# Kernel tuning notes

Hardware: AMD Instinct MI355X
Metric: run time of the kernel (lower is better)

## Reference

```python
import jax, jax.numpy as jnp
import numpy as np

B, S, UC = 64, 5, 50          # batch, sample (candidates), clicked history
D, T = 128, 768               # embedding_size, title_size
NE, NR, NN = 200000, 100, 50000  # entities, relations, news
K, A = 10, 20                 # neighbors per entity, anchor nodes per news


def _lin(k, out_d, in_d):
    w = jax.random.normal(k, (out_d, in_d), jnp.float32) * (1.0 / np.sqrt(in_d))
    b = jnp.zeros((out_d,), jnp.float32)
    return w, b


def setup_inputs() -> dict:
    key = jax.random.key(0)
    ks = jax.random.split(key, 16)
    W_nc1, b_nc1 = _lin(ks[0], D, T)
    W_nc2, b_nc2 = _lin(ks[1], D, D)
    W_anchor, b_anchor = _lin(ks[2], D, 2 * D)
    W_aw1, b_aw1 = _lin(ks[3], D, D)
    W_aw2, b_aw2 = _lin(ks[4], 1, D)
    W_mlp1, b_mlp1 = _lin(ks[5], D, 2 * D)
    W_mlp2, b_mlp2 = _lin(ks[6], D, D)
    return {
        "news_title_embedding": jax.random.normal(ks[7], (NN, T), jnp.float32),
        "entity_embedding": jax.random.normal(ks[8], (NE, D), jnp.float32),
        "relation_embedding": jax.random.normal(ks[9], (NR, D), jnp.float32),
        "W_nc1": W_nc1, "b_nc1": b_nc1, "W_nc2": W_nc2, "b_nc2": b_nc2,
        "W_anchor": W_anchor, "b_anchor": b_anchor,
        "W_aw1": W_aw1, "b_aw1": b_aw1, "W_aw2": W_aw2, "b_aw2": b_aw2,
        "W_mlp1": W_mlp1, "b_mlp1": b_mlp1, "W_mlp2": W_mlp2, "b_mlp2": b_mlp2,
        "cand_news": jax.random.randint(ks[10], (B, S), 0, NN, jnp.int32),
        "clicked_news": jax.random.randint(ks[11], (B, UC), 0, NN, jnp.int32),
        "cand_anchor_nodes": jax.random.randint(ks[12], (B * S, A), 0, NE, jnp.int32),
        "clicked_anchor_nodes": jax.random.randint(ks[13], (B * UC, A), 0, NE, jnp.int32),
        "entity_adj": jax.random.randint(ks[14], (NE, K), 0, NE, jnp.int32),
        "relation_adj": jax.random.randint(ks[15], (NE, K), 0, NR, jnp.int32),
    }


def reference(news_title_embedding, entity_embedding, relation_embedding,
              W_nc1, b_nc1, W_nc2, b_nc2,
              W_anchor, b_anchor, W_aw1, b_aw1, W_aw2, b_aw2,
              W_mlp1, b_mlp1, W_mlp2, b_mlp2,
              cand_news, clicked_news, cand_anchor_nodes, clicked_anchor_nodes,
              entity_adj, relation_adj):
    elu = jax.nn.elu

    def news_emb(ids_flat):  # [N] -> [N, D]
        t = news_title_embedding[ids_flat]                       # [N, T]
        return jnp.tanh(elu(t @ W_nc1.T + b_nc1) @ W_nc2.T + b_nc2)

    def anchor_graph_emb(nodes):  # [N, A] -> [N, D]
        node_e = entity_embedding[nodes]                          # [N, A, D]
        nb_ent = entity_embedding[entity_adj[nodes]]              # [N, A, K, D]
        nb_rel = relation_embedding[relation_adj[nodes]]          # [N, A, K, D]
        agg = jnp.sum(nb_ent + nb_rel, axis=-2)                   # [N, A, D]
        h = jnp.tanh(jnp.concatenate([node_e, agg], axis=-1) @ W_anchor.T + b_anchor)
        logits = elu(h @ W_aw1.T + b_aw1) @ W_aw2.T + b_aw2       # [N, A, 1]
        w = jax.nn.softmax(logits, axis=-2)                       # softmax over anchor nodes
        return jnp.sum(h * w, axis=-2)                            # [N, D]

    cand_e = news_emb(cand_news.reshape(-1))                      # [B*S, D]
    clk_e = news_emb(clicked_news.reshape(-1))                    # [B*UC, D]
    cand_e = jnp.concatenate([cand_e, anchor_graph_emb(cand_anchor_nodes)], axis=-1)
    clk_e = jnp.concatenate([clk_e, anchor_graph_emb(clicked_anchor_nodes)], axis=-1)

    def mlp(x):
        return elu(elu(x @ W_mlp1.T + b_mlp1) @ W_mlp2.T + b_mlp2)

    news_embedding = mlp(cand_e).reshape(B, S, -1)                # [B, S, D]
    user_embedding = jnp.mean(mlp(clk_e).reshape(B, UC, -1), axis=1)  # [B, D]
    score = jnp.sum(news_embedding * user_embedding[:, None, :], axis=-1)  # [B, S]
    return score
```

## Files before the change

kernel.cpp:

```cpp
#include <hip/hip_runtime.h>
#include <hip/hip_bf16.h>


#define B_ 64
#define S_ 5
#define UC_ 50
#define A_ 20
#define NCAND 320
#define NCLK 3200
#define NNEWS 3520
#define NANCH 70400

static constexpr long OFF_WNC1P = 64;
static constexpr long OFF_BNC1  = 98368;
static constexpr long OFF_WNC2P = 98496;
static constexpr long OFF_BNC2  = 114880;
static constexpr long OFF_WANCP = 115008;
static constexpr long OFF_BANC  = 147776;
static constexpr long OFF_WAW1P = 147904;
static constexpr long OFF_BAW1  = 164288;
static constexpr long OFF_WAW2  = 164416;
static constexpr long OFF_BAW2  = 164544;
static constexpr long OFF_WM1P  = 164548;
static constexpr long OFF_BM1   = 197316;
static constexpr long OFF_WM2P  = 197444;
static constexpr long OFF_BM2   = 213828;
static constexpr long OFF_REL   = 213956;
static constexpr long OFF_AE    = 226756;
static constexpr long OFF_NE    = 677316;
static constexpr long OFF_MO    = 1127876;

typedef __attribute__((ext_vector_type(8))) short short8v;
typedef __attribute__((ext_vector_type(4))) float f32x4;

__device__ __forceinline__ float ldf(const void* p, long i, int bf) {
  if (bf) {
    unsigned int u = (unsigned int)((const unsigned short*)p)[i];
    u <<= 16;
    return __uint_as_float(u);
  }
  return ((const float*)p)[i];
}

__device__ __forceinline__ float4 ldf4(const void* p, long i, int bf) {
  float4 f;
  if (bf) {
    const unsigned short* q = (const unsigned short*)p + i;
    uint2 u = *(const uint2*)q;
    f.x = __uint_as_float(u.x << 16);
    f.y = __uint_as_float(u.x & 0xffff0000u);
    f.z = __uint_as_float(u.y << 16);
    f.w = __uint_as_float(u.y & 0xffff0000u);
  } else {
    f = *(const float4*)((const float*)p + i);
  }
  return f;
}

__device__ __forceinline__ float eluf(float v) { return v > 0.f ? v : expm1f(v); }

__device__ __forceinline__ void splitbf(float v, unsigned short& hi, unsigned short& lo) {
  unsigned int b = __float_as_uint(v);
  hi = (unsigned short)(b >> 16);
  float rm = v - __uint_as_float(b & 0xffff0000u);
  unsigned int rb = __float_as_uint(rm);
  lo = (unsigned short)((rb + 0x7fffu + ((rb >> 16) & 1u)) >> 16);
}

__device__ __forceinline__ float bfh(unsigned short u) {
  return __uint_as_float((unsigned int)u << 16);
}

__global__ void k_detect(const void* ent, int* flag) {
  __shared__ int cnt;
  if (threadIdx.x == 0) cnt = 0;
  __syncthreads();
  unsigned short u = ((const unsigned short*)ent)[threadIdx.x];
  int e = (u >> 7) & 0xFF;
  int ok = (e >= 107 && e <= 146) ? 1 : 0;
  atomicAdd(&cnt, ok);
  __syncthreads();
  if (threadIdx.x == 0) *flag = (cnt >= 200) ? 1 : 0;
}

__global__ __launch_bounds__(256) void k_prep(
    const void* s0, const void* s1, const void* s2, const void* s3,
    const void* s4, const void* s5, const void* s6, const void* s7,
    const void* s8, const void* s9, const void* s10, const void* s11,
    const void* s12, const void* s13, const void* s14, float* ws) {
  const int bf = ((const int*)ws)[0];
  const void* srcs[15] = {s0,s1,s2,s3,s4,s5,s6,s7,s8,s9,s10,s11,s12,s13,s14};
  const int R[15] = {128,128,128,128,128,128,128,128,1,  1,  128,128,128,128,100};
  const int C[15] = {768,1,  128,1,  256,1,  128,1,  128,1,  256,1,  128,1,  128};
  const int MD[15]= {2,  0,  2,  0,  3,  0,  3,  0,  0,  0,  2,  0,  2,  0,  0};
  const long OFF[15] = {OFF_WNC1P,OFF_BNC1,OFF_WNC2P,OFF_BNC2,OFF_WANCP,OFF_BANC,
                        OFF_WAW1P,OFF_BAW1,OFF_WAW2,OFF_BAW2,OFF_WM1P,OFF_BM1,
                        OFF_WM2P,OFF_BM2,OFF_REL};
  const long total = 226689;
  for (long idx = (long)blockIdx.x * blockDim.x + threadIdx.x; idx < total;
       idx += (long)gridDim.x * blockDim.x) {
    long rem = idx;
    int s = 0;
    while (rem >= (long)R[s] * C[s]) { rem -= (long)R[s] * C[s]; s++; }
    float v = ldf(srcs[s], rem, bf);
    if (MD[s] == 2) {
      long r = rem / C[s], c = rem - r * C[s];
      ws[OFF[s] + (c >> 2) * 512 + r * 4 + (c & 3)] = v;
    } else if (MD[s] == 3) {
      long r = rem / C[s], c = rem - r * C[s];
      unsigned short hi, lo;
      splitbf(v, hi, lo);
      unsigned short* H = (unsigned short*)(ws + OFF[s]);
      unsigned short* L = H + (s == 4 ? 32768 : 16384);
      long id2 = ((c >> 5) * 128 + r) * 32 + (c & 31);
      H[id2] = hi;
      L[id2] = lo;
    } else {
      ws[OFF[s] + rem] = v;
    }
  }
}

__global__ __launch_bounds__(128) void k_news(const void* titles, const int* cand,
                                              const int* clk, float* ws) {
  const int bf = ((const int*)ws)[0];
  __shared__ __align__(16) float t[8][768];
  __shared__ __align__(16) float h1[8][128];
  int tid = threadIdx.x;
  long r0 = (long)blockIdx.x * 8;
  for (int x = tid * 4; x < 8 * 768; x += 128 * 4) {
    int c = x / 768, k = x - c * 768;
    long i = r0 + c;
    int id = (i < NCAND) ? cand[i] : clk[i - NCAND];
    *(float4*)&t[c][k] = ldf4(titles, (long)id * 768 + k, bf);
  }
  __syncthreads();
  int j = tid;
  const float4* W1 = (const float4*)(ws + OFF_WNC1P);
  float acc[8];
#pragma unroll
  for (int c = 0; c < 8; c++) acc[c] = 0.f;
  for (int k4 = 0; k4 < 192; k4++) {
    float4 w = W1[k4 * 128 + j];
#pragma unroll
    for (int c = 0; c < 8; c++) {
      const float4 xv = *(const float4*)&t[c][k4 * 4];
      acc[c] += w.x * xv.x + w.y * xv.y + w.z * xv.z + w.w * xv.w;
    }
  }
  float b1 = ws[OFF_BNC1 + j];
#pragma unroll
  for (int c = 0; c < 8; c++) h1[c][j] = eluf(acc[c] + b1);
  __syncthreads();
  const float4* W2 = (const float4*)(ws + OFF_WNC2P);
  float a2[8];
#pragma unroll
  for (int c = 0; c < 8; c++) a2[c] = 0.f;
  for (int k4 = 0; k4 < 32; k4++) {
    float4 w = W2[k4 * 128 + j];
#pragma unroll
    for (int c = 0; c < 8; c++) {
      const float4 xv = *(const float4*)&h1[c][k4 * 4];
      a2[c] += w.x * xv.x + w.y * xv.y + w.z * xv.z + w.w * xv.w;
    }
  }
  float b2 = ws[OFF_BNC2 + j];
  float* NE = ws + OFF_NE;
#pragma unroll
  for (int c = 0; c < 8; c++) NE[(r0 + c) * 128 + j] = tanhf(a2[c] + b2);
}

__global__ __launch_bounds__(256, 2) void k_anchor(const void* ent, const int* canda,
                                                   const int* clka, const int* eadj,
                                                   const int* radj, float* ws) {
  __shared__ __align__(16) unsigned short XbH[16][264];
  __shared__ __align__(16) unsigned short XbL[16][264];
  __shared__ __align__(16) unsigned short Hhi[80][136];
  __shared__ __align__(16) unsigned short Hlo[80][136];
  __shared__ int NodeIdL[80];
  __shared__ int EAdjL[800];
  __shared__ int RAdjL[800];
  __shared__ float LGp[4][80];

  const int bf = ((const int*)ws)[0];
  int tid = threadIdx.x;
  int lane = tid & 63, wv = tid >> 6;
  int r16 = lane & 15, khh = lane >> 4;
  int lane32 = tid & 31, grp = tid >> 5;
  const float* relf = ws + OFF_REL;

  const unsigned short* WAH = (const unsigned short*)(ws + OFF_WANCP);
  const unsigned short* WAL = WAH + 32768;
  const unsigned short* W1H = (const unsigned short*)(ws + OFF_WAW1P);
  const unsigned short* W1L = W1H + 16384;

  if (tid < 80) {
    long n = (long)blockIdx.x * 80 + tid;
    NodeIdL[tid] = (n < (long)NCAND * A_) ? canda[n] : clka[n - (long)NCAND * A_];
  }
  __syncthreads();
  for (int t = tid; t < 800; t += 256) {
    int rr = t / 10, kk = t - rr * 10;
    int nd = NodeIdL[rr];
    EAdjL[t] = eadj[(long)nd * 10 + kk];
    RAdjL[t] = radj[(long)nd * 10 + kk];
  }
  __syncthreads();

  for (int mt = 0; mt < 5; ++mt) {
    for (int i = 0; i < 2; ++i) {
      int cr = grp * 2 + i;
      int gr = mt * 16 + cr;
      int node = NodeIdL[gr];
      float4 x1 = ldf4(ent, (long)node * 128 + lane32 * 4, bf);
      float4 a = {0.f, 0.f, 0.f, 0.f};
#pragma unroll
      for (int k = 0; k < 10; ++k) {
        int an = EAdjL[gr * 10 + k], rn = RAdjL[gr * 10 + k];
        float4 e = ldf4(ent, (long)an * 128 + lane32 * 4, bf);
        const float4 r = *(const float4*)&relf[(long)rn * 128 + lane32 * 4];
        a.x += e.x + r.x;
        a.y += e.y + r.y;
        a.z += e.z + r.z;
        a.w += e.w + r.w;
      }
      ushort4 h4, l4;
      splitbf(x1.x, h4.x, l4.x); splitbf(x1.y, h4.y, l4.y);
      splitbf(x1.z, h4.z, l4.z); splitbf(x1.w, h4.w, l4.w);
      *(ushort4*)&XbH[cr][lane32 * 4] = h4;
      *(ushort4*)&XbL[cr][lane32 * 4] = l4;
      splitbf(a.x, h4.x, l4.x); splitbf(a.y, h4.y, l4.y);
      splitbf(a.z, h4.z, l4.z); splitbf(a.w, h4.w, l4.w);
      *(ushort4*)&XbH[cr][128 + lane32 * 4] = h4;
      *(ushort4*)&XbL[cr][128 + lane32 * 4] = l4;
    }
    __syncthreads();

    {
      f32x4 acc0 = {}, acc1 = {};
      int n0 = wv * 32 + r16, n1 = n0 + 16;
      for (int kt = 0; kt < 8; ++kt) {
        short8v ahi = *(const short8v*)&XbH[r16][kt * 32 + khh * 8];
        short8v alo = *(const short8v*)&XbL[r16][kt * 32 + khh * 8];
        long w0 = ((long)(kt * 128 + n0)) * 32 + khh * 8;
        long w1 = ((long)(kt * 128 + n1)) * 32 + khh * 8;
        short8v b0h = *(const short8v*)(WAH + w0);
        short8v b0l = *(const short8v*)(WAL + w0);
        short8v b1h = *(const short8v*)(WAH + w1);
        short8v b1l = *(const short8v*)(WAL + w1);
        acc0 = __builtin_amdgcn_mfma_f32_16x16x32_bf16(ahi, b0h, acc0, 0, 0, 0);
        acc0 = __builtin_amdgcn_mfma_f32_16x16x32_bf16(ahi, b0l, acc0, 0, 0, 0);
        acc0 = __builtin_amdgcn_mfma_f32_16x16x32_bf16(alo, b0h, acc0, 0, 0, 0);
        acc1 = __builtin_amdgcn_mfma_f32_16x16x32_bf16(ahi, b1h, acc1, 0, 0, 0);
        acc1 = __builtin_amdgcn_mfma_f32_16x16x32_bf16(ahi, b1l, acc1, 0, 0, 0);
        acc1 = __builtin_amdgcn_mfma_f32_16x16x32_bf16(alo, b1h, acc1, 0, 0, 0);
      }
      float bc0 = ws[OFF_BANC + n0], bc1 = ws[OFF_BANC + n1];
#pragma unroll
      for (int j = 0; j < 4; ++j) {
        int r = mt * 16 + khh * 4 + j;
        unsigned short hi, lo;
        float h0 = tanhf(acc0[j] + bc0);
        splitbf(h0, hi, lo);
        Hhi[r][n0] = hi; Hlo[r][n0] = lo;
        float h1 = tanhf(acc1[j] + bc1);
        splitbf(h1, hi, lo);
        Hhi[r][n1] = hi; Hlo[r][n1] = lo;
      }
    }
    __syncthreads();
  }

  {
    int n0 = wv * 32 + r16, n1 = n0 + 16;
    float b10 = ws[OFF_BAW1 + n0], b11 = ws[OFF_BAW1 + n1];
    float w20 = ws[OFF_WAW2 + n0], w21 = ws[OFF_WAW2 + n1];
    for (int mt = 0; mt < 5; ++mt) {
      f32x4 ac0 = {}, ac1 = {};
      for (int kt = 0; kt < 4; ++kt) {
        short8v ahi = *(const short8v*)&Hhi[mt * 16 + r16][kt * 32 + khh * 8];
        short8v alo = *(const short8v*)&Hlo[mt * 16 + r16][kt * 32 + khh * 8];
        long w0 = ((long)(kt * 128 + n0)) * 32 + khh * 8;
        long w1 = ((long)(kt * 128 + n1)) * 32 + khh * 8;
        short8v b0h = *(const short8v*)(W1H + w0);
        short8v b0l = *(const short8v*)(W1L + w0);
        short8v b1h = *(const short8v*)(W1H + w1);
        short8v b1l = *(const short8v*)(W1L + w1);
        ac0 = __builtin_amdgcn_mfma_f32_16x16x32_bf16(ahi, b0h, ac0, 0, 0, 0);
        ac0 = __builtin_amdgcn_mfma_f32_16x16x32_bf16(ahi, b0l, ac0, 0, 0, 0);
        ac0 = __builtin_amdgcn_mfma_f32_16x16x32_bf16(alo, b0h, ac0, 0, 0, 0);
        ac1 = __builtin_amdgcn_mfma_f32_16x16x32_bf16(ahi, b1h, ac1, 0, 0, 0);
        ac1 = __builtin_amdgcn_mfma_f32_16x16x32_bf16(ahi, b1l, ac1, 0, 0, 0);
        ac1 = __builtin_amdgcn_mfma_f32_16x16x32_bf16(alo, b1h, ac1, 0, 0, 0);
      }
#pragma unroll
      for (int j = 0; j < 4; ++j) {
        float v = eluf(ac0[j] + b10) * w20 + eluf(ac1[j] + b11) * w21;
        v += __shfl_xor(v, 1);
        v += __shfl_xor(v, 2);
        v += __shfl_xor(v, 4);
        v += __shfl_xor(v, 8);
        if (r16 == 0) LGp[wv][mt * 16 + khh * 4 + j] = v;
      }
    }
  }
  __syncthreads();

  {
    int g = tid >> 6, ar = g * 20;
    float bw2 = ws[OFF_BAW2];
    float e[20], mx = -1e30f;
#pragma unroll
    for (int a = 0; a < 20; ++a) {
      int rr = ar + a;
      e[a] = LGp[0][rr] + LGp[1][rr] + LGp[2][rr] + LGp[3][rr] + bw2;
      mx = fmaxf(mx, e[a]);
    }
    float s = 0.f;
#pragma unroll
    for (int a = 0; a < 20; ++a) { e[a] = expf(e[a] - mx); s += e[a]; }
    float inv = 1.0f / s;
    float o0 = 0.f, o1 = 0.f;
#pragma unroll
    for (int a = 0; a < 20; ++a) {
      int rr = ar + a;
      float w = e[a];
      o0 += w * (bfh(Hhi[rr][lane]) + bfh(Hlo[rr][lane]));
      o1 += w * (bfh(Hhi[rr][lane + 64]) + bfh(Hlo[rr][lane + 64]));
    }
    float* AE = ws + OFF_AE;
    long ro = ((long)blockIdx.x * 4 + g) * 128;
    AE[ro + lane]      = o0 * inv;
    AE[ro + lane + 64] = o1 * inv;
  }
}

__global__ __launch_bounds__(256) void k_mlp(float* ws) {
  __shared__ __align__(16) float xt[16][256];
  __shared__ __align__(16) float h1[16][128];
  int tid = threadIdx.x;
  long r0 = (long)blockIdx.x * 16;
  const float* NE = ws + OFF_NE;
  const float* AE = ws + OFF_AE;
  for (int x = tid; x < 16 * 256; x += 256) {
    int c = x >> 8, k = x & 255;
    xt[c][k] = (k < 128) ? NE[(r0 + c) * 128 + k] : AE[(r0 + c) * 128 + (k - 128)];
  }
  __syncthreads();
  int j = tid & 127, half = tid >> 7;
  const float4* W1 = (const float4*)(ws + OFF_WM1P);
  float acc[8];
#pragma unroll
  for (int c = 0; c < 8; c++) acc[c] = 0.f;
  for (int k4 = 0; k4 < 64; k4++) {
    float4 w = W1[k4 * 128 + j];
#pragma unroll
    for (int c = 0; c < 8; c++) {
      const float4 xv = *(const float4*)&xt[half * 8 + c][k4 * 4];
      acc[c] += w.x * xv.x + w.y * xv.y + w.z * xv.z + w.w * xv.w;
    }
  }
  float b1 = ws[OFF_BM1 + j];
#pragma unroll
  for (int c = 0; c < 8; c++) h1[half * 8 + c][j] = eluf(acc[c] + b1);
  __syncthreads();
  const float4* W2 = (const float4*)(ws + OFF_WM2P);
  float a2[8];
#pragma unroll
  for (int c = 0; c < 8; c++) a2[c] = 0.f;
  for (int k4 = 0; k4 < 32; k4++) {
    float4 w = W2[k4 * 128 + j];
#pragma unroll
    for (int c = 0; c < 8; c++) {
      const float4 xv = *(const float4*)&h1[half * 8 + c][k4 * 4];
      a2[c] += w.x * xv.x + w.y * xv.y + w.z * xv.z + w.w * xv.w;
    }
  }
  float b2 = ws[OFF_BM2 + j];
  float* MO = ws + OFF_MO;
#pragma unroll
  for (int c = 0; c < 8; c++) MO[(r0 + half * 8 + c) * 128 + j] = eluf(a2[c] + b2);
}

__global__ __launch_bounds__(128) void k_score(const float* ws, void* out) {
  const int bf = ((const int*)ws)[0];
  int b = blockIdx.x;
  int d = threadIdx.x;
  const float* MO = ws + OFF_MO;
  float u = 0.f;
  for (int t = 0; t < UC_; t++) u += MO[(long)(NCAND + b * UC_ + t) * 128 + d];
  u *= (1.0f / UC_);
  __shared__ float red[2];
  for (int s = 0; s < S_; s++) {
    float p = MO[(long)(b * S_ + s) * 128 + d] * u;
#pragma unroll
    for (int o = 32; o > 0; o >>= 1) p += __shfl_down(p, o, 64);
    if ((d & 63) == 0) red[d >> 6] = p;
    __syncthreads();
    if (d == 0) {
      float v = red[0] + red[1];
      if (bf)
        ((__hip_bfloat16*)out)[b * S_ + s] = __float2bfloat16(v);
      else
        ((float*)out)[b * S_ + s] = v;
    }
    __syncthreads();
  }
}

extern "C" void kernel_launch(void* const* d_in, const int* in_sizes, int n_in,
                              void* d_out, int out_size, void* d_ws, size_t ws_size,
                              hipStream_t stream) {
  (void)in_sizes; (void)n_in; (void)out_size; (void)ws_size;
  const void* titles = d_in[0];
  const void* ent    = d_in[1];
  const void* rel    = d_in[2];
  const void* Wnc1 = d_in[3];  const void* bnc1 = d_in[4];
  const void* Wnc2 = d_in[5];  const void* bnc2 = d_in[6];
  const void* Wanc = d_in[7];  const void* banc = d_in[8];
  const void* Waw1 = d_in[9];  const void* baw1 = d_in[10];
  const void* Waw2 = d_in[11]; const void* baw2 = d_in[12];
  const void* Wm1  = d_in[13]; const void* bm1  = d_in[14];
  const void* Wm2  = d_in[15]; const void* bm2  = d_in[16];
  const int* cand  = (const int*)d_in[17];
  const int* clk   = (const int*)d_in[18];
  const int* canda = (const int*)d_in[19];
  const int* clka  = (const int*)d_in[20];
  const int* eadj  = (const int*)d_in[21];
  const int* radj  = (const int*)d_in[22];
  float* ws = (float*)d_ws;

  k_detect<<<1, 256, 0, stream>>>(ent, (int*)d_ws);
  k_prep<<<256, 256, 0, stream>>>(Wnc1, bnc1, Wnc2, bnc2, Wanc, banc, Waw1, baw1,
                                  Waw2, baw2, Wm1, bm1, Wm2, bm2, rel, ws);
  k_news<<<NNEWS / 8, 128, 0, stream>>>(titles, cand, clk, ws);
  k_anchor<<<NANCH / 80, 256, 0, stream>>>(ent, canda, clka, eadj, radj, ws);
  k_mlp<<<NNEWS / 16, 256, 0, stream>>>(ws);
  k_score<<<B_, 128, 0, stream>>>(ws, d_out);
}
```

Baseline: 230.4 us.

## Process one news item per anchor block to raise block count and occupancy

```diff
diff --git a/kernel.cpp b/kernel.cpp
--- a/kernel.cpp
+++ b/kernel.cpp
@@ -170,17 +170,17 @@
   for (int c = 0; c < 8; c++) NE[(r0 + c) * 128 + j] = tanhf(a2[c] + b2);
 }
 
-__global__ __launch_bounds__(256, 2) void k_anchor(const void* ent, const int* canda,
+__global__ __launch_bounds__(256, 3) void k_anchor(const void* ent, const int* canda,
                                                    const int* clka, const int* eadj,
                                                    const int* radj, float* ws) {
-  __shared__ __align__(16) unsigned short XbH[16][264];
-  __shared__ __align__(16) unsigned short XbL[16][264];
-  __shared__ __align__(16) unsigned short Hhi[80][136];
-  __shared__ __align__(16) unsigned short Hlo[80][136];
-  __shared__ int NodeIdL[80];
-  __shared__ int EAdjL[800];
-  __shared__ int RAdjL[800];
-  __shared__ float LGp[4][80];
+  __shared__ __align__(16) unsigned short XbH[32][264];
+  __shared__ __align__(16) unsigned short XbL[32][264];
+  __shared__ __align__(16) unsigned short Hhi[32][136];
+  __shared__ __align__(16) unsigned short Hlo[32][136];
+  __shared__ int NodeIdL[20];
+  __shared__ int EAdjL[200];
+  __shared__ int RAdjL[200];
+  __shared__ float LGp[4][20];
 
   const int bf = ((const int*)ws)[0];
   int tid = threadIdx.x;
@@ -194,29 +194,29 @@
   const unsigned short* W1H = (const unsigned short*)(ws + OFF_WAW1P);
   const unsigned short* W1L = W1H + 16384;
 
-  if (tid < 80) {
-    long n = (long)blockIdx.x * 80 + tid;
+  if (tid < 20) {
+    long n = (long)blockIdx.x * 20 + tid;
     NodeIdL[tid] = (n < (long)NCAND * A_) ? canda[n] : clka[n - (long)NCAND * A_];
   }
   __syncthreads();
-  for (int t = tid; t < 800; t += 256) {
-    int rr = t / 10, kk = t - rr * 10;
+  if (tid < 200) {
+    int rr = tid / 10, kk = tid - rr * 10;
     int nd = NodeIdL[rr];
-    EAdjL[t] = eadj[(long)nd * 10 + kk];
-    RAdjL[t] = radj[(long)nd * 10 + kk];
-  }
-  __syncthreads();
-
-  for (int mt = 0; mt < 5; ++mt) {
-    for (int i = 0; i < 2; ++i) {
-      int cr = grp * 2 + i;
-      int gr = mt * 16 + cr;
-      int node = NodeIdL[gr];
+    EAdjL[tid] = eadj[(long)nd * 10 + kk];
+    RAdjL[tid] = radj[(long)nd * 10 + kk];
+  }
+  __syncthreads();
+
+#pragma unroll
+  for (int i = 0; i < 3; ++i) {
+    int row = grp + i * 8;
+    if (row < 20) {
+      int node = NodeIdL[row];
       float4 x1 = ldf4(ent, (long)node * 128 + lane32 * 4, bf);
       float4 a = {0.f, 0.f, 0.f, 0.f};
 #pragma unroll
       for (int k = 0; k < 10; ++k) {
-        int an = EAdjL[gr * 10 + k], rn = RAdjL[gr * 10 + k];
+        int an = EAdjL[row * 10 + k], rn = RAdjL[row * 10 + k];
         float4 e = ldf4(ent, (long)an * 128 + lane32 * 4, bf);
         const float4 r = *(const float4*)&relf[(long)rn * 128 + lane32 * 4];
         a.x += e.x + r.x;
@@ -227,111 +227,114 @@
       ushort4 h4, l4;
       splitbf(x1.x, h4.x, l4.x); splitbf(x1.y, h4.y, l4.y);
       splitbf(x1.z, h4.z, l4.z); splitbf(x1.w, h4.w, l4.w);
-      *(ushort4*)&XbH[cr][lane32 * 4] = h4;
-      *(ushort4*)&XbL[cr][lane32 * 4] = l4;
+      *(ushort4*)&XbH[row][lane32 * 4] = h4;
+      *(ushort4*)&XbL[row][lane32 * 4] = l4;
       splitbf(a.x, h4.x, l4.x); splitbf(a.y, h4.y, l4.y);
       splitbf(a.z, h4.z, l4.z); splitbf(a.w, h4.w, l4.w);
-      *(ushort4*)&XbH[cr][128 + lane32 * 4] = h4;
-      *(ushort4*)&XbL[cr][128 + lane32 * 4] = l4;
-    }
-    __syncthreads();
-
-    {
-      f32x4 acc0 = {}, acc1 = {};
-      int n0 = wv * 32 + r16, n1 = n0 + 16;
-      for (int kt = 0; kt < 8; ++kt) {
-        short8v ahi = *(const short8v*)&XbH[r16][kt * 32 + khh * 8];
-        short8v alo = *(const short8v*)&XbL[r16][kt * 32 + khh * 8];
-        long w0 = ((long)(kt * 128 + n0)) * 32 + khh * 8;
-        long w1 = ((long)(kt * 128 + n1)) * 32 + khh * 8;
-        short8v b0h = *(const short8v*)(WAH + w0);
-        short8v b0l = *(const short8v*)(WAL + w0);
-        short8v b1h = *(const short8v*)(WAH + w1);
-        short8v b1l = *(const short8v*)(WAL + w1);
-        acc0 = __builtin_amdgcn_mfma_f32_16x16x32_bf16(ahi, b0h, acc0, 0, 0, 0);
-        acc0 = __builtin_amdgcn_mfma_f32_16x16x32_bf16(ahi, b0l, acc0, 0, 0, 0);
-        acc0 = __builtin_amdgcn_mfma_f32_16x16x32_bf16(alo, b0h, acc0, 0, 0, 0);
-        acc1 = __builtin_amdgcn_mfma_f32_16x16x32_bf16(ahi, b1h, acc1, 0, 0, 0);
-        acc1 = __builtin_amdgcn_mfma_f32_16x16x32_bf16(ahi, b1l, acc1, 0, 0, 0);
-        acc1 = __builtin_amdgcn_mfma_f32_16x16x32_bf16(alo, b1h, acc1, 0, 0, 0);
+      *(ushort4*)&XbH[row][128 + lane32 * 4] = h4;
+      *(ushort4*)&XbL[row][128 + lane32 * 4] = l4;
+    }
+  }
+  __syncthreads();
+
+  {
+    int n0 = wv * 32 + r16, n1 = n0 + 16;
+    f32x4 acc[2][2] = {};
+    for (int kt = 0; kt < 8; ++kt) {
+      long w0 = ((long)(kt * 128 + n0)) * 32 + khh * 8;
+      long w1 = ((long)(kt * 128 + n1)) * 32 + khh * 8;
+      short8v b0h = *(const short8v*)(WAH + w0);
+      short8v b0l = *(const short8v*)(WAL + w0);
+      short8v b1h = *(const short8v*)(WAH + w1);
+      short8v b1l = *(const short8v*)(WAL + w1);
+#pragma unroll
+      for (int mt = 0; mt < 2; ++mt) {
+        short8v ahi = *(const short8v*)&XbH[mt * 16 + r16][kt * 32 + khh * 8];
+        short8v alo = *(const short8v*)&XbL[mt * 16 + r16][kt * 32 + khh * 8];
+        acc[mt][0] = __builtin_amdgcn_mfma_f32_16x16x32_bf16(ahi, b0h, acc[mt][0], 0, 0, 0);
+        acc[mt][0] = __builtin_amdgcn_mfma_f32_16x16x32_bf16(ahi, b0l, acc[mt][0], 0, 0, 0);
+        acc[mt][0] = __builtin_amdgcn_mfma_f32_16x16x32_bf16(alo, b0h, acc[mt][0], 0, 0, 0);
+        acc[mt][1] = __builtin_amdgcn_mfma_f32_16x16x32_bf16(ahi, b1h, acc[mt][1], 0, 0, 0);
+        acc[mt][1] = __builtin_amdgcn_mfma_f32_16x16x32_bf16(ahi, b1l, acc[mt][1], 0, 0, 0);
+        acc[mt][1] = __builtin_amdgcn_mfma_f32_16x16x32_bf16(alo, b1h, acc[mt][1], 0, 0, 0);
       }
-      float bc0 = ws[OFF_BANC + n0], bc1 = ws[OFF_BANC + n1];
+    }
+    float bc0 = ws[OFF_BANC + n0], bc1 = ws[OFF_BANC + n1];
+#pragma unroll
+    for (int mt = 0; mt < 2; ++mt)
 #pragma unroll
       for (int j = 0; j < 4; ++j) {
         int r = mt * 16 + khh * 4 + j;
-        unsigned short hi, lo;
-        float h0 = tanhf(acc0[j] + bc0);
-        splitbf(h0, hi, lo);
-        Hhi[r][n0] = hi; Hlo[r][n0] = lo;
-        float h1 = tanhf(acc1[j] + bc1);
-        splitbf(h1, hi, lo);
-        Hhi[r][n1] = hi; Hlo[r][n1] = lo;
+        if (r < 20) {
+          unsigned short hi, lo;
+          float h0 = tanhf(acc[mt][0][j] + bc0);
+          splitbf(h0, hi, lo);
+          Hhi[r][n0] = hi; Hlo[r][n0] = lo;
+          float h1 = tanhf(acc[mt][1][j] + bc1);
+          splitbf(h1, hi, lo);
+          Hhi[r][n1] = hi; Hlo[r][n1] = lo;
+        }
       }
-    }
-    __syncthreads();
-  }
+  }
+  __syncthreads();
 
   {
     int n0 = wv * 32 + r16, n1 = n0 + 16;
     float b10 = ws[OFF_BAW1 + n0], b11 = ws[OFF_BAW1 + n1];
     float w20 = ws[OFF_WAW2 + n0], w21 = ws[OFF_WAW2 + n1];
-    for (int mt = 0; mt < 5; ++mt) {
-      f32x4 ac0 = {}, ac1 = {};
-      for (int kt = 0; kt < 4; ++kt) {
+    f32x4 ac[2][2] = {};
+    for (int kt = 0; kt < 4; ++kt) {
+      long w0 = ((long)(kt * 128 + n0)) * 32 + khh * 8;
+      long w1 = ((long)(kt * 128 + n1)) * 32 + khh * 8;
+      short8v b0h = *(const short8v*)(W1H + w0);
+      short8v b0l = *(const short8v*)(W1L + w0);
+      short8v b1h = *(const short8v*)(W1H + w1);
+      short8v b1l = *(const short8v*)(W1L + w1);
+#pragma unroll
+      for (int mt = 0; mt < 2; ++mt) {
         short8v ahi = *(const short8v*)&Hhi[mt * 16 + r16][kt * 32 + khh * 8];
         short8v alo = *(const short8v*)&Hlo[mt * 16 + r16][kt * 32 + khh * 8];
-        long w0 = ((long)(kt * 128 + n0)) * 32 + khh * 8;
-        long w1 = ((long)(kt * 128 + n1)) * 32 + khh * 8;
-        short8v b0h = *(const short8v*)(W1H + w0);
-        short8v b0l = *(const short8v*)(W1L + w0);
-        short8v b1h = *(const short8v*)(W1H + w1);
-        short8v b1l = *(const short8v*)(W1L + w1);
-        ac0 = __builtin_amdgcn_mfma_f32_16x16x32_bf16(ahi, b0h, ac0, 0, 0, 0);
-        ac0 = __builtin_amdgcn_mfma_f32_16x16x32_bf16(ahi, b0l, ac0, 0, 0, 0);
-        ac0 = __builtin_amdgcn_mfma_f32_16x16x32_bf16(alo, b0h, ac0, 0, 0, 0);
-        ac1 = __builtin_amdgcn_mfma_f32_16x16x32_bf16(ahi, b1h, ac1, 0, 0, 0);
-        ac1 = __builtin_amdgcn_mfma_f32_16x16x32_bf16(ahi, b1l, ac1, 0, 0, 0);
-        ac1 = __builtin_amdgcn_mfma_f32_16x16x32_bf16(alo, b1h, ac1, 0, 0, 0);
+        ac[mt][0] = __builtin_amdgcn_mfma_f32_16x16x32_bf16(ahi, b0h, ac[mt][0], 0, 0, 0);
+        ac[mt][0] = __builtin_amdgcn_mfma_f32_16x16x32_bf16(ahi, b0l, ac[mt][0], 0, 0, 0);
+        ac[mt][0] = __builtin_amdgcn_mfma_f32_16x16x32_bf16(alo, b0h, ac[mt][0], 0, 0, 0);
+        ac[mt][1] = __builtin_amdgcn_mfma_f32_16x16x32_bf16(ahi, b1h, ac[mt][1], 0, 0, 0);
+        ac[mt][1] = __builtin_amdgcn_mfma_f32_16x16x32_bf16(ahi, b1l, ac[mt][1], 0, 0, 0);
+        ac[mt][1] = __builtin_amdgcn_mfma_f32_16x16x32_bf16(alo, b1h, ac[mt][1], 0, 0, 0);
       }
+    }
+#pragma unroll
+    for (int mt = 0; mt < 2; ++mt)
 #pragma unroll
       for (int j = 0; j < 4; ++j) {
-        float v = eluf(ac0[j] + b10) * w20 + eluf(ac1[j] + b11) * w21;
+        float v = eluf(ac[mt][0][j] + b10) * w20 + eluf(ac[mt][1][j] + b11) * w21;
         v += __shfl_xor(v, 1);
         v += __shfl_xor(v, 2);
         v += __shfl_xor(v, 4);
         v += __shfl_xor(v, 8);
-        if (r16 == 0) LGp[wv][mt * 16 + khh * 4 + j] = v;
+        int r = mt * 16 + khh * 4 + j;
+        if (r16 == 0 && r < 20) LGp[wv][r] = v;
       }
-    }
-  }
-  __syncthreads();
-
-  {
-    int g = tid >> 6, ar = g * 20;
+  }
+  __syncthreads();
+
+  if (tid < 128) {
     float bw2 = ws[OFF_BAW2];
     float e[20], mx = -1e30f;
 #pragma unroll
     for (int a = 0; a < 20; ++a) {
-      int rr = ar + a;
-      e[a] = LGp[0][rr] + LGp[1][rr] + LGp[2][rr] + LGp[3][rr] + bw2;
+      e[a] = LGp[0][a] + LGp[1][a] + LGp[2][a] + LGp[3][a] + bw2;
       mx = fmaxf(mx, e[a]);
     }
     float s = 0.f;
 #pragma unroll
     for (int a = 0; a < 20; ++a) { e[a] = expf(e[a] - mx); s += e[a]; }
     float inv = 1.0f / s;
-    float o0 = 0.f, o1 = 0.f;
-#pragma unroll
-    for (int a = 0; a < 20; ++a) {
-      int rr = ar + a;
-      float w = e[a];
-      o0 += w * (bfh(Hhi[rr][lane]) + bfh(Hlo[rr][lane]));
-      o1 += w * (bfh(Hhi[rr][lane + 64]) + bfh(Hlo[rr][lane + 64]));
-    }
+    float o = 0.f;
+#pragma unroll
+    for (int a = 0; a < 20; ++a)
+      o += e[a] * (bfh(Hhi[a][tid]) + bfh(Hlo[a][tid]));
     float* AE = ws + OFF_AE;
-    long ro = ((long)blockIdx.x * 4 + g) * 128;
-    AE[ro + lane]      = o0 * inv;
-    AE[ro + lane + 64] = o1 * inv;
+    AE[(long)blockIdx.x * 128 + tid] = o * inv;
   }
 }
 
@@ -434,7 +437,7 @@
   k_prep<<<256, 256, 0, stream>>>(Wnc1, bnc1, Wnc2, bnc2, Wanc, banc, Waw1, baw1,
                                   Waw2, baw2, Wm1, bm1, Wm2, bm2, rel, ws);
   k_news<<<NNEWS / 8, 128, 0, stream>>>(titles, cand, clk, ws);
-  k_anchor<<<NANCH / 80, 256, 0, stream>>>(ent, canda, clka, eadj, radj, ws);
+  k_anchor<<<NNEWS, 256, 0, stream>>>(ent, canda, clka, eadj, radj, ws);
   k_mlp<<<NNEWS / 16, 256, 0, stream>>>(ws);
   k_score<<<B_, 128, 0, stream>>>(ws, d_out);
 }
```

Result: faster. 224.2 us (-2.7%).
